# Optimization experiments

Measured on AMD Instinct MI355X. Metric: run time of the kernel, lower is better.

## Reference

```python
import jax, jax.numpy as jnp
import numpy as np

N = 50000        # nodes
E = 1_600_000    # edges (avg degree 32)
IN, HID, OUT = 128, 64, 16


def setup_inputs() -> dict:
    key = jax.random.key(0)
    k0, k1, k2, k3, k4 = jax.random.split(key, 5)
    src = jax.random.randint(k0, (E,), 0, N, dtype=jnp.int32)
    dst = jax.random.randint(k1, (E,), 0, N, dtype=jnp.int32)
    features = jax.random.normal(k2, (N, IN), dtype=jnp.float32)
    W1 = jax.random.normal(k3, (IN, HID), dtype=jnp.float32) / np.float32(np.sqrt(IN))
    b1 = jnp.zeros((HID,), jnp.float32)
    W2 = jax.random.normal(k4, (HID, OUT), dtype=jnp.float32) / np.float32(np.sqrt(HID))
    b2 = jnp.zeros((OUT,), jnp.float32)
    return {"features": features, "W1": W1, "b1": b1, "W2": W2, "b2": b2,
            "src": src, "dst": dst}


def _graph_conv(src, dst, x, W, b):
    # DGL GraphConv, norm='both':  out = D_dst^{-1/2} * A^T * (D_src^{-1/2} * x) @ W + b
    ones = jnp.ones((src.shape[0],), x.dtype)
    deg_out = jax.ops.segment_sum(ones, src, num_segments=N)  # out-degree of source nodes
    deg_in = jax.ops.segment_sum(ones, dst, num_segments=N)   # in-degree of dest nodes
    norm_s = jax.lax.rsqrt(jnp.maximum(deg_out, 1.0))
    norm_d = jax.lax.rsqrt(jnp.maximum(deg_in, 1.0))
    # project first (in_feats >= out_feats) so messages are in the smaller dim
    h = (x * norm_s[:, None]) @ W                              # [N, out_dim]
    agg = jax.ops.segment_sum(h[src], dst, num_segments=N)     # sparse aggregate
    return agg * norm_d[:, None] + b


def reference(features, W1, b1, W2, b2, src, dst):
    h = jax.nn.relu(_graph_conv(src, dst, features, W1, b1))
    return _graph_conv(src, dst, h, W2, b2)
```

## Files before the change

kernel.cpp:

```cpp
#include <hip/hip_runtime.h>
#include <hip/hip_fp16.h>

#define IN_F  128
#define HID_F 64
#define OUT_F 16
#define MAX_N 50176
#define HWORDS (MAX_N / 2)
#define QWORDS (MAX_N / 4)
#define NSEG  256

#define SCAN_BLOCK 256
#define SCAN_CHUNK 1024

#define LSTR 136
#define XSTR 68

typedef __attribute__((ext_vector_type(8))) _Float16 half8;
typedef __attribute__((ext_vector_type(4))) _Float16 half4v;
typedef __attribute__((ext_vector_type(4))) float    floatx4;

__global__ __launch_bounds__(1024) void hist2_kernel(const int* __restrict__ src,
                                                     const int* __restrict__ dst,
                                                     unsigned int* __restrict__ partial,
                                                     int E, int seg, int Wr8) {
    __shared__ unsigned int cnt[QWORDS];
    int b = blockIdx.x;
    const int* ids = blockIdx.y ? dst : src;
    unsigned int* pbase = partial + (size_t)blockIdx.y * NSEG * Wr8;
    for (int w = threadIdx.x; w < Wr8; w += 1024) cnt[w] = 0;
    __syncthreads();
    int lo = b * seg, hi = min(lo + seg, E);
    for (int e = lo + threadIdx.x; e < hi; e += 1024) {
        int d = ids[e];
        atomicAdd(&cnt[d >> 2], 1u << ((d & 3) * 8));
    }
    __syncthreads();
    for (int w = threadIdx.x; w < Wr8; w += 1024)
        pbase[(size_t)b * Wr8 + w] = cnt[w];
}

__global__ __launch_bounds__(256) void reduce_norm_kernel(unsigned int* __restrict__ partial,
                                                          int* __restrict__ row_start,
                                                          int* __restrict__ bsum,
                                                          float* __restrict__ norm_s,
                                                          float* __restrict__ norm_d,
                                                          int Wr8, int N) {
    int t = threadIdx.x;
    int w = blockIdx.x * 256 + t;
    if (blockIdx.y == 0) {
        if (w >= Wr8) return;
        unsigned int r0 = 0, r1 = 0, r2 = 0, r3 = 0;
        const unsigned int* base = partial;
        for (int b = 0; b < NSEG; b++) {
            unsigned int v = base[(size_t)b * Wr8 + w];
            r0 += v & 0xFFu; r1 += (v >> 8) & 0xFFu;
            r2 += (v >> 16) & 0xFFu; r3 += v >> 24;
        }
        int d = 4 * w;
        if (d     < N) norm_s[d]     = rsqrtf(fmaxf((float)r0, 1.0f));
        if (d + 1 < N) norm_s[d + 1] = rsqrtf(fmaxf((float)r1, 1.0f));
        if (d + 2 < N) norm_s[d + 2] = rsqrtf(fmaxf((float)r2, 1.0f));
        if (d + 3 < N) norm_s[d + 3] = rsqrtf(fmaxf((float)r3, 1.0f));
        return;
    }
    __shared__ int part[256];
    bool inr = (w < Wr8);
    unsigned int r0 = 0, r1 = 0, r2 = 0, r3 = 0;
    if (inr) {
        unsigned int* base = partial + (size_t)NSEG * Wr8;
        for (int b = 0; b < NSEG; b++) {
            size_t idx = (size_t)b * Wr8 + w;
            unsigned int v = base[idx];
            base[idx] = r0 | (r1 << 8) | (r2 << 16) | (r3 << 24);
            r0 += v & 0xFFu; r1 += (v >> 8) & 0xFFu;
            r2 += (v >> 16) & 0xFFu; r3 += v >> 24;
        }
        int d = 4 * w;
        if (d     < N) norm_d[d]     = rsqrtf(fmaxf((float)r0, 1.0f));
        if (d + 1 < N) norm_d[d + 1] = rsqrtf(fmaxf((float)r1, 1.0f));
        if (d + 2 < N) norm_d[d + 2] = rsqrtf(fmaxf((float)r2, 1.0f));
        if (d + 3 < N) norm_d[d + 3] = rsqrtf(fmaxf((float)r3, 1.0f));
    }
    part[t] = inr ? (int)(r0 + r1 + r2 + r3) : 0;
    __syncthreads();
    for (int off = 1; off < 256; off <<= 1) {
        int x = (t >= off) ? part[t - off] : 0;
        __syncthreads();
        part[t] += x;
        __syncthreads();
    }
    if (inr) {
        int run = (t > 0) ? part[t - 1] : 0;
        int d = 4 * w;
        if (d     < N) row_start[d]     = run;
        run += (int)r0;
        if (d + 1 < N) row_start[d + 1] = run;
        run += (int)r1;
        if (d + 2 < N) row_start[d + 2] = run;
        run += (int)r2;
        if (d + 3 < N) row_start[d + 3] = run;
    }
    if (t == 255) bsum[blockIdx.x] = part[255];
}

__global__ __launch_bounds__(1024) void scan_bsum_kernel(int* __restrict__ bsum, int nblocks) {
    __shared__ int part[1024];
    int t = threadIdx.x;
    int v = (t < nblocks) ? bsum[t] : 0;
    part[t] = v;
    __syncthreads();
    for (int off = 1; off < 1024; off <<= 1) {
        int x = (t >= off) ? part[t - off] : 0;
        __syncthreads();
        part[t] += x;
        __syncthreads();
    }
    if (t < nblocks) bsum[t] = part[t] - v;
}

__global__ __launch_bounds__(1024) void scatter_lds_kernel(const int* __restrict__ src,
                                                           const int* __restrict__ dst,
                                                           const int* __restrict__ row_start,
                                                           const int* __restrict__ bsum,
                                                           const unsigned int* __restrict__ prefix,
                                                           unsigned short* __restrict__ csr_src,
                                                           int E, int seg, int Wr8, int N,
                                                           int nchunks) {
    __shared__ unsigned int pos[HWORDS];
    __shared__ int sbsum[64];
    int b = blockIdx.x;
    int t = threadIdx.x;
    if (t < 64) sbsum[t] = (t < nchunks) ? bsum[t] : 0;
    int half = (N + 1) >> 1;
    for (int w = t; w < half; w += 1024) {
        int d0 = 2 * w, d1 = 2 * w + 1;
        unsigned int word = prefix[(size_t)b * Wr8 + (w >> 1)];
        unsigned int b0 = (word >> ((d0 & 3) * 8)) & 0xFFu;
        unsigned int b1 = (word >> ((d1 & 3) * 8)) & 0xFFu;
        unsigned int lo = (unsigned int)row_start[d0] + b0;
        unsigned int hi = (d1 < N) ? ((unsigned int)row_start[d1] + b1) : 0u;
        pos[w] = lo | (hi << 16);
    }
    __syncthreads();
    int lo = b * seg, hiE = min(lo + seg, E);
    for (int e = lo + t; e < hiE; e += 1024) {
        int d = dst[e];
        unsigned int sh = (unsigned int)(d & 1) * 16u;
        unsigned int old = atomicAdd(&pos[d >> 1], 1u << sh);
        unsigned int q = (old >> sh) & 0xFFFFu;
        csr_src[q + (unsigned int)sbsum[d >> 10]] = (unsigned short)src[e];
    }
}

__global__ __launch_bounds__(256) void gemm1_kernel(const float* __restrict__ x,
                                                    const float* __restrict__ W,
                                                    const float* __restrict__ norm_s,
                                                    __half* __restrict__ h, int N) {
    __shared__ _Float16 sx[64 * LSTR];
    __shared__ _Float16 sw[64 * LSTR];
    int t = threadIdx.x;
    int row0 = blockIdx.x * 64;

    for (int i = t; i < IN_F * 16; i += 256) {
        int k = i >> 4, n4 = (i & 15) * 4;
        float4 w4 = *(const float4*)(W + (size_t)k * HID_F + n4);
        sw[(n4 + 0) * LSTR + k] = (_Float16)w4.x;
        sw[(n4 + 1) * LSTR + k] = (_Float16)w4.y;
        sw[(n4 + 2) * LSTR + k] = (_Float16)w4.z;
        sw[(n4 + 3) * LSTR + k] = (_Float16)w4.w;
    }
    for (int i = t; i < 64 * 32; i += 256) {
        int r = i >> 5, k4 = (i & 31) * 4;
        int gr = row0 + r;
        half4v hv = {0, 0, 0, 0};
        if (gr < N) {
            float4 v = *(const float4*)(x + (size_t)gr * IN_F + k4);
            float ns = norm_s[gr];
            hv.x = (_Float16)(v.x * ns); hv.y = (_Float16)(v.y * ns);
            hv.z = (_Float16)(v.z * ns); hv.w = (_Float16)(v.w * ns);
        }
        *(half4v*)(sx + r * LSTR + k4) = hv;
    }
    __syncthreads();

    int wave = t >> 6, lane = t & 63;
    int m = lane & 15, quad = lane >> 4;
    int rbase = wave * 16;

    floatx4 acc[4] = {{0,0,0,0}, {0,0,0,0}, {0,0,0,0}, {0,0,0,0}};
    #pragma unroll
    for (int ks = 0; ks < 4; ks++) {
        half8 av = *(half8*)(sx + (rbase + m) * LSTR + ks * 32 + quad * 8);
        #pragma unroll
        for (int ct = 0; ct < 4; ct++) {
            half8 bv = *(half8*)(sw + (ct * 16 + m) * LSTR + ks * 32 + quad * 8);
            acc[ct] = __builtin_amdgcn_mfma_f32_16x16x32_f16(av, bv, acc[ct], 0, 0, 0);
        }
    }
    #pragma unroll
    for (int ct = 0; ct < 4; ct++) {
        #pragma unroll
        for (int reg = 0; reg < 4; reg++) {
            int gr = row0 + rbase + quad * 4 + reg;
            if (gr < N) h[(size_t)gr * HID_F + ct * 16 + m] = __float2half(acc[ct][reg]);
        }
    }
}

__global__ __launch_bounds__(256) void agg1_kernel(const int* __restrict__ row_start,
                                                   const int* __restrict__ bsum,
                                                   const unsigned short* __restrict__ csr_src,
                                                   const __half* __restrict__ h,
                                                   const float* __restrict__ norm_d,
                                                   const float* __restrict__ norm_s,
                                                   const float* __restrict__ b1,
                                                   const float* __restrict__ W2,
                                                   __half* __restrict__ h2, int N, int E) {
    __shared__ float sW2T[OUT_F][XSTR];
    __shared__ float xrow[16][XSTR];
    int t = threadIdx.x;
    for (int i = t; i < HID_F * OUT_F; i += 256) {
        int k = i >> 4, o = i & 15;
        sW2T[o][k] = W2[i];
    }

    int wave = t >> 6, lane = t & 63;
    int slot = lane >> 3;
    int fh   = lane & 7;
    int nbase = blockIdx.x * 16 + wave * 4;

    int rs[5];
    #pragma unroll
    for (int j = 0; j < 5; j++) {
        int n = nbase + j;
        rs[j] = (n < N) ? (row_start[n] + bsum[n >> 10]) : E;
    }

    #pragma unroll
    for (int nn = 0; nn < 4; nn++) {
        int node = nbase + nn;
        if (node < N) {
            int beg = rs[nn], end = rs[nn + 1];

            float f[8] = {0.f, 0.f, 0.f, 0.f, 0.f, 0.f, 0.f, 0.f};

            #define AGG1_BODY(SIDX) {                                                  \
                const uint4* p = (const uint4*)(h + (size_t)(SIDX) * HID_F + fh * 8);  \
                uint4 u = *p;                                                          \
                __half2 q0 = *(__half2*)&u.x, q1 = *(__half2*)&u.y;                    \
                __half2 q2 = *(__half2*)&u.z, q3 = *(__half2*)&u.w;                    \
                float2 g0 = __half22float2(q0), g1 = __half22float2(q1);               \
                float2 g2 = __half22float2(q2), g3 = __half22float2(q3);               \
                f[0] += g0.x; f[1] += g0.y; f[2] += g1.x; f[3] += g1.y;                \
                f[4] += g2.x; f[5] += g2.y; f[6] += g3.x; f[7] += g3.y; }

            int i = beg + slot;
            for (; i + 24 < end; i += 32) {
                int s0 = (int)csr_src[i];
                int s1 = (int)csr_src[i + 8];
                int s2 = (int)csr_src[i + 16];
                int s3 = (int)csr_src[i + 24];
                AGG1_BODY(s0); AGG1_BODY(s1); AGG1_BODY(s2); AGG1_BODY(s3);
            }
            for (; i < end; i += 8) {
                int s = (int)csr_src[i];
                AGG1_BODY(s);
            }
            #undef AGG1_BODY

            #pragma unroll
            for (int j = 0; j < 8; j++) {
                f[j] += __shfl_xor(f[j], 8);
                f[j] += __shfl_xor(f[j], 16);
                f[j] += __shfl_xor(f[j], 32);
            }

            if (slot == 0) {
                float nd = norm_d[node], ns = norm_s[node];
                const float4 bA = *(const float4*)(b1 + fh * 8);
                const float4 bB = *(const float4*)(b1 + fh * 8 + 4);
                float4 vA, vB;
                vA.x = fmaxf(f[0] * nd + bA.x, 0.f) * ns;
                vA.y = fmaxf(f[1] * nd + bA.y, 0.f) * ns;
                vA.z = fmaxf(f[2] * nd + bA.z, 0.f) * ns;
                vA.w = fmaxf(f[3] * nd + bA.w, 0.f) * ns;
                vB.x = fmaxf(f[4] * nd + bB.x, 0.f) * ns;
                vB.y = fmaxf(f[5] * nd + bB.y, 0.f) * ns;
                vB.z = fmaxf(f[6] * nd + bB.z, 0.f) * ns;
                vB.w = fmaxf(f[7] * nd + bB.w, 0.f) * ns;
                *(float4*)&xrow[wave * 4 + nn][fh * 8]     = vA;
                *(float4*)&xrow[wave * 4 + nn][fh * 8 + 4] = vB;
            }
        }
    }
    __syncthreads();

    int nr = t >> 4, o = t & 15;
    int gnode = blockIdx.x * 16 + nr;
    if (gnode < N) {
        float acc = 0.0f;
        #pragma unroll
        for (int k4 = 0; k4 < HID_F / 4; k4++) {
            float4 x4 = *(const float4*)&xrow[nr][k4 * 4];
            float4 w4 = *(const float4*)&sW2T[o][k4 * 4];
            acc += x4.x * w4.x + x4.y * w4.y + x4.z * w4.z + x4.w * w4.w;
        }
        h2[(size_t)gnode * OUT_F + o] = __float2half(acc);
    }
}

__global__ __launch_bounds__(256) void agg2_kernel(const int* __restrict__ row_start,
                                                   const int* __restrict__ bsum,
                                                   const unsigned short* __restrict__ csr_src,
                                                   const __half* __restrict__ h2,
                                                   const float* __restrict__ norm_d,
                                                   const float* __restrict__ b2,
                                                   float* __restrict__ out, int N, int E) {
    int node = blockIdx.x * 4 + (threadIdx.x >> 6);
    if (node >= N) return;
    int lane = threadIdx.x & 63;
    int slot = lane >> 2;
    int fh   = lane & 3;
    int beg = row_start[node] + bsum[node >> 10];
    int end = (node + 1 < N) ? row_start[node + 1] + bsum[(node + 1) >> 10] : E;

    float f0 = 0.f, f1 = 0.f, f2 = 0.f, f3 = 0.f;

    #define AGG2_BODY(SIDX) {                                                  \
        const uint2* p = (const uint2*)(h2 + (size_t)(SIDX) * OUT_F + fh * 4); \
        uint2 u = *p;                                                          \
        __half2 q0 = *(__half2*)&u.x, q1 = *(__half2*)&u.y;                    \
        float2 g0 = __half22float2(q0), g1 = __half22float2(q1);               \
        f0 += g0.x; f1 += g0.y; f2 += g1.x; f3 += g1.y; }

    int i = beg + slot;
    for (; i + 16 < end; i += 32) {
        int s0 = (int)csr_src[i];
        int s1 = (int)csr_src[i + 16];
        AGG2_BODY(s0); AGG2_BODY(s1);
    }
    if (i < end) {
        int s = (int)csr_src[i];
        AGG2_BODY(s);
    }
    #undef AGG2_BODY

    f0 += __shfl_xor(f0, 4);  f1 += __shfl_xor(f1, 4);
    f2 += __shfl_xor(f2, 4);  f3 += __shfl_xor(f3, 4);
    f0 += __shfl_xor(f0, 8);  f1 += __shfl_xor(f1, 8);
    f2 += __shfl_xor(f2, 8);  f3 += __shfl_xor(f3, 8);
    f0 += __shfl_xor(f0, 16); f1 += __shfl_xor(f1, 16);
    f2 += __shfl_xor(f2, 16); f3 += __shfl_xor(f3, 16);
    f0 += __shfl_xor(f0, 32); f1 += __shfl_xor(f1, 32);
    f2 += __shfl_xor(f2, 32); f3 += __shfl_xor(f3, 32);

    if (slot == 0) {
        float nd = norm_d[node];
        float4 v;
        v.x = f0 * nd + b2[fh * 4 + 0];
        v.y = f1 * nd + b2[fh * 4 + 1];
        v.z = f2 * nd + b2[fh * 4 + 2];
        v.w = f3 * nd + b2[fh * 4 + 3];
        *(float4*)(out + (size_t)node * OUT_F + fh * 4) = v;
    }
}

extern "C" void kernel_launch(void* const* d_in, const int* in_sizes, int n_in,
                              void* d_out, int out_size, void* d_ws, size_t ws_size,
                              hipStream_t stream) {
    const float* feat = (const float*)d_in[0];
    const float* W1   = (const float*)d_in[1];
    const float* b1   = (const float*)d_in[2];
    const float* W2   = (const float*)d_in[3];
    const float* b2   = (const float*)d_in[4];
    const int*   src  = (const int*)d_in[5];
    const int*   dst  = (const int*)d_in[6];

    const int N   = in_sizes[0] / IN_F;
    const int E   = in_sizes[5];
    const int seg = (E + NSEG - 1) / NSEG;
    const int Wr8 = (N + 3) >> 2;
    const int nchunks = (N + SCAN_CHUNK - 1) / SCAN_CHUNK;

    float* fws    = (float*)d_ws;
    float* norm_s = fws;
    float* norm_d = fws + N;
    __half* h1    = (__half*)(fws + 2 * (size_t)N);
    __half* h2    = h1 + (size_t)N * HID_F;
    int*   iws    = (int*)(h2 + (size_t)N * OUT_F);
    int*   row_start = iws;
    int*   bsum      = iws + N + 1;
    unsigned int* partial = (unsigned int*)(iws + N + 1 + 1024);
    unsigned short* csr_src = (unsigned short*)(partial + 2 * (size_t)NSEG * Wr8);

    hist2_kernel<<<dim3(NSEG, 2), 1024, 0, stream>>>(src, dst, partial, E, seg, Wr8);
    reduce_norm_kernel<<<dim3((Wr8 + 255) / 256, 2), 256, 0, stream>>>(partial, row_start, bsum, norm_s, norm_d, Wr8, N);
    scan_bsum_kernel<<<1, 1024, 0, stream>>>(bsum, nchunks);

    scatter_lds_kernel<<<NSEG, 1024, 0, stream>>>(src, dst, row_start, bsum,
                                                  partial + (size_t)NSEG * Wr8,
                                                  csr_src, E, seg, Wr8, N, nchunks);

    gemm1_kernel<<<(N + 63) / 64, 256, 0, stream>>>(feat, W1, norm_s, h1, N);
    agg1_kernel<<<(N + 15) / 16, 256, 0, stream>>>(row_start, bsum, csr_src, h1, norm_d, norm_s, b1, W2, h2, N, E);
    agg2_kernel<<<(N + 3) / 4, 256, 0, stream>>>(row_start, bsum, csr_src, h2, norm_d, b2, (float*)d_out, N, E);
}
```

Measured before the change: 224.8 us.

## Parallelize degree reduction across segments with wave shuffles and split row scan

Replaces the per-thread serial loop over 256 histogram segments with one wavefront per pair of packed columns. Each lane handles four segments and the wave combines them with shuffle reductions and scans, while still writing per-segment exclusive offsets for the scatter. The row_start prefix scan moves into a separate small kernel using wave-level shuffles. This exposes far more parallelism than the old under-occupied kernel, at the cost of an extra launch and strided, less coalesced global reads.

```diff
diff --git a/kernel.cpp b/kernel.cpp
--- a/kernel.cpp
+++ b/kernel.cpp
@@ -9,7 +9,6 @@
 #define QWORDS (MAX_N / 4)
 #define NSEG  256
 
-#define SCAN_BLOCK 256
 #define SCAN_CHUNK 1024
 
 #define LSTR 136
@@ -39,68 +38,129 @@
         pbase[(size_t)b * Wr8 + w] = cnt[w];
 }
 
-__global__ __launch_bounds__(256) void reduce_norm_kernel(unsigned int* __restrict__ partial,
-                                                          int* __restrict__ row_start,
-                                                          int* __restrict__ bsum,
-                                                          float* __restrict__ norm_s,
-                                                          float* __restrict__ norm_d,
-                                                          int Wr8, int N) {
+__global__ __launch_bounds__(256) void reduce_norm2_kernel(unsigned int* __restrict__ partial,
+                                                           unsigned int* __restrict__ wsum,
+                                                           float* __restrict__ norm_s,
+                                                           float* __restrict__ norm_d,
+                                                           int Wr8, int N) {
+    int wave = threadIdx.x >> 6, lane = threadIdx.x & 63;
+    int p = blockIdx.x * 4 + wave;
+    int w0 = 2 * p;
+    if (w0 >= Wr8) return;
+    bool pair = (w0 + 1 < Wr8);
+
+    if (blockIdx.y == 0) {
+        const unsigned int* base = partial;
+        unsigned int s0 = 0, s1 = 0;
+        #pragma unroll
+        for (int j = 0; j < 4; j++) {
+            size_t idx = (size_t)(4 * lane + j) * Wr8 + w0;
+            if (pair) { uint2 v = *(const uint2*)(base + idx); s0 += v.x; s1 += v.y; }
+            else      { s0 += base[idx]; }
+        }
+        #pragma unroll
+        for (int off = 1; off < 64; off <<= 1) {
+            s0 += __shfl_xor(s0, off);
+            s1 += __shfl_xor(s1, off);
+        }
+        if (lane == 0) {
+            int d = 4 * w0;
+            if (d     < N) norm_s[d]     = rsqrtf(fmaxf((float)( s0        & 0xFFu), 1.0f));
+            if (d + 1 < N) norm_s[d + 1] = rsqrtf(fmaxf((float)((s0 >>  8) & 0xFFu), 1.0f));
+            if (d + 2 < N) norm_s[d + 2] = rsqrtf(fmaxf((float)((s0 >> 16) & 0xFFu), 1.0f));
+            if (d + 3 < N) norm_s[d + 3] = rsqrtf(fmaxf((float)( s0 >> 24        ), 1.0f));
+            if (pair) {
+                if (d + 4 < N) norm_s[d + 4] = rsqrtf(fmaxf((float)( s1        & 0xFFu), 1.0f));
+                if (d + 5 < N) norm_s[d + 5] = rsqrtf(fmaxf((float)((s1 >>  8) & 0xFFu), 1.0f));
+                if (d + 6 < N) norm_s[d + 6] = rsqrtf(fmaxf((float)((s1 >> 16) & 0xFFu), 1.0f));
+                if (d + 7 < N) norm_s[d + 7] = rsqrtf(fmaxf((float)( s1 >> 24        ), 1.0f));
+            }
+        }
+        return;
+    }
+
+    unsigned int* base = partial + (size_t)NSEG * Wr8;
+    unsigned int a0[4], a1[4];
+    #pragma unroll
+    for (int j = 0; j < 4; j++) {
+        size_t idx = (size_t)(4 * lane + j) * Wr8 + w0;
+        if (pair) { uint2 v = *(const uint2*)(base + idx); a0[j] = v.x; a1[j] = v.y; }
+        else      { a0[j] = base[idx]; a1[j] = 0u; }
+    }
+    unsigned int e0[4], e1[4], l0 = 0, l1 = 0;
+    #pragma unroll
+    for (int j = 0; j < 4; j++) {
+        e0[j] = l0; l0 += a0[j];
+        e1[j] = l1; l1 += a1[j];
+    }
+    unsigned int inc0 = l0, inc1 = l1;
+    #pragma unroll
+    for (int off = 1; off < 64; off <<= 1) {
+        unsigned int v0 = __shfl_up(inc0, off);
+        unsigned int v1 = __shfl_up(inc1, off);
+        if (lane >= off) { inc0 += v0; inc1 += v1; }
+    }
+    unsigned int exc0 = __shfl_up(inc0, 1);
+    unsigned int exc1 = __shfl_up(inc1, 1);
+    if (lane == 0) { exc0 = 0; exc1 = 0; }
+    #pragma unroll
+    for (int j = 0; j < 4; j++) {
+        size_t idx = (size_t)(4 * lane + j) * Wr8 + w0;
+        if (pair) { uint2 v; v.x = exc0 + e0[j]; v.y = exc1 + e1[j]; *(uint2*)(base + idx) = v; }
+        else      { base[idx] = exc0 + e0[j]; }
+    }
+    unsigned int tot0 = __shfl(inc0, 63);
+    unsigned int tot1 = __shfl(inc1, 63);
+    if (lane == 0) {
+        wsum[w0] = tot0;
+        if (pair) wsum[w0 + 1] = tot1;
+        int d = 4 * w0;
+        if (d     < N) norm_d[d]     = rsqrtf(fmaxf((float)( tot0        & 0xFFu), 1.0f));
+        if (d + 1 < N) norm_d[d + 1] = rsqrtf(fmaxf((float)((tot0 >>  8) & 0xFFu), 1.0f));
+        if (d + 2 < N) norm_d[d + 2] = rsqrtf(fmaxf((float)((tot0 >> 16) & 0xFFu), 1.0f));
+        if (d + 3 < N) norm_d[d + 3] = rsqrtf(fmaxf((float)( tot0 >> 24        ), 1.0f));
+        if (pair) {
+            if (d + 4 < N) norm_d[d + 4] = rsqrtf(fmaxf((float)( tot1        & 0xFFu), 1.0f));
+            if (d + 5 < N) norm_d[d + 5] = rsqrtf(fmaxf((float)((tot1 >>  8) & 0xFFu), 1.0f));
+            if (d + 6 < N) norm_d[d + 6] = rsqrtf(fmaxf((float)((tot1 >> 16) & 0xFFu), 1.0f));
+            if (d + 7 < N) norm_d[d + 7] = rsqrtf(fmaxf((float)( tot1 >> 24        ), 1.0f));
+        }
+    }
+}
+
+__global__ __launch_bounds__(256) void scan_local_kernel(const unsigned int* __restrict__ wsum,
+                                                         int* __restrict__ row_start,
+                                                         int* __restrict__ bsum,
+                                                         int Wr8, int N) {
+    __shared__ int wsums[4];
     int t = threadIdx.x;
+    int wave = t >> 6, lane = t & 63;
     int w = blockIdx.x * 256 + t;
-    if (blockIdx.y == 0) {
-        if (w >= Wr8) return;
-        unsigned int r0 = 0, r1 = 0, r2 = 0, r3 = 0;
-        const unsigned int* base = partial;
-        for (int b = 0; b < NSEG; b++) {
-            unsigned int v = base[(size_t)b * Wr8 + w];
-            r0 += v & 0xFFu; r1 += (v >> 8) & 0xFFu;
-            r2 += (v >> 16) & 0xFFu; r3 += v >> 24;
-        }
-        int d = 4 * w;
-        if (d     < N) norm_s[d]     = rsqrtf(fmaxf((float)r0, 1.0f));
-        if (d + 1 < N) norm_s[d + 1] = rsqrtf(fmaxf((float)r1, 1.0f));
-        if (d + 2 < N) norm_s[d + 2] = rsqrtf(fmaxf((float)r2, 1.0f));
-        if (d + 3 < N) norm_s[d + 3] = rsqrtf(fmaxf((float)r3, 1.0f));
-        return;
-    }
-    __shared__ int part[256];
-    bool inr = (w < Wr8);
-    unsigned int r0 = 0, r1 = 0, r2 = 0, r3 = 0;
-    if (inr) {
-        unsigned int* base = partial + (size_t)NSEG * Wr8;
-        for (int b = 0; b < NSEG; b++) {
-            size_t idx = (size_t)b * Wr8 + w;
-            unsigned int v = base[idx];
-            base[idx] = r0 | (r1 << 8) | (r2 << 16) | (r3 << 24);
-            r0 += v & 0xFFu; r1 += (v >> 8) & 0xFFu;
-            r2 += (v >> 16) & 0xFFu; r3 += v >> 24;
-        }
-        int d = 4 * w;
-        if (d     < N) norm_d[d]     = rsqrtf(fmaxf((float)r0, 1.0f));
-        if (d + 1 < N) norm_d[d + 1] = rsqrtf(fmaxf((float)r1, 1.0f));
-        if (d + 2 < N) norm_d[d + 2] = rsqrtf(fmaxf((float)r2, 1.0f));
-        if (d + 3 < N) norm_d[d + 3] = rsqrtf(fmaxf((float)r3, 1.0f));
-    }
-    part[t] = inr ? (int)(r0 + r1 + r2 + r3) : 0;
-    __syncthreads();
-    for (int off = 1; off < 256; off <<= 1) {
-        int x = (t >= off) ? part[t - off] : 0;
-        __syncthreads();
-        part[t] += x;
-        __syncthreads();
-    }
-    if (inr) {
-        int run = (t > 0) ? part[t - 1] : 0;
-        int d = 4 * w;
-        if (d     < N) row_start[d]     = run;
-        run += (int)r0;
-        if (d + 1 < N) row_start[d + 1] = run;
-        run += (int)r1;
-        if (d + 2 < N) row_start[d + 2] = run;
-        run += (int)r2;
-        if (d + 3 < N) row_start[d + 3] = run;
-    }
-    if (t == 255) bsum[blockIdx.x] = part[255];
+    unsigned int v = (w < Wr8) ? wsum[w] : 0u;
+    int c0 = (int)(v & 0xFFu), c1 = (int)((v >> 8) & 0xFFu);
+    int c2 = (int)((v >> 16) & 0xFFu), c3 = (int)(v >> 24);
+    int s = c0 + c1 + c2 + c3;
+    int inc = s;
+    #pragma unroll
+    for (int off = 1; off < 64; off <<= 1) {
+        int x = __shfl_up(inc, off);
+        if (lane >= off) inc += x;
+    }
+    if (lane == 63) wsums[wave] = inc;
+    __syncthreads();
+    int woff = 0;
+    #pragma unroll
+    for (int k = 0; k < 4; k++) woff += (k < wave) ? wsums[k] : 0;
+    int run = woff + inc - s;
+    int d = 4 * w;
+    if (d     < N) row_start[d]     = run;
+    run += c0;
+    if (d + 1 < N) row_start[d + 1] = run;
+    run += c1;
+    if (d + 2 < N) row_start[d + 2] = run;
+    run += c2;
+    if (d + 3 < N) row_start[d + 3] = run;
+    if (t == 0) bsum[blockIdx.x] = wsums[0] + wsums[1] + wsums[2] + wsums[3];
 }
 
 __global__ __launch_bounds__(1024) void scan_bsum_kernel(int* __restrict__ bsum, int nblocks) {
@@ -381,6 +441,7 @@
     const int seg = (E + NSEG - 1) / NSEG;
     const int Wr8 = (N + 3) >> 2;
     const int nchunks = (N + SCAN_CHUNK - 1) / SCAN_CHUNK;
+    const int npairs  = (Wr8 + 1) >> 1;
 
     float* fws    = (float*)d_ws;
     float* norm_s = fws;
@@ -390,11 +451,13 @@
     int*   iws    = (int*)(h2 + (size_t)N * OUT_F);
     int*   row_start = iws;
     int*   bsum      = iws + N + 1;
-    unsigned int* partial = (unsigned int*)(iws + N + 1 + 1024);
+    unsigned int* wsum = (unsigned int*)(iws + N + 1 + 1024);
+    unsigned int* partial = wsum + Wr8;
     unsigned short* csr_src = (unsigned short*)(partial + 2 * (size_t)NSEG * Wr8);
 
     hist2_kernel<<<dim3(NSEG, 2), 1024, 0, stream>>>(src, dst, partial, E, seg, Wr8);
-    reduce_norm_kernel<<<dim3((Wr8 + 255) / 256, 2), 256, 0, stream>>>(partial, row_start, bsum, norm_s, norm_d, Wr8, N);
+    reduce_norm2_kernel<<<dim3((npairs + 3) / 4, 2), 256, 0, stream>>>(partial, wsum, norm_s, norm_d, Wr8, N);
+    scan_local_kernel<<<nchunks, 256, 0, stream>>>(wsum, row_start, bsum, Wr8, N);
     scan_bsum_kernel<<<1, 1024, 0, stream>>>(bsum, nchunks);
 
     scatter_lds_kernel<<<NSEG, 1024, 0, stream>>>(src, dst, row_start, bsum,
```

After: 223.7 us. Within noise of the previous version (-0.5%).
